# Kernel optimization log

Hardware: AMD Instinct MI355X
Metric: run time of the kernel (lower is better)

## Reference

```python
import jax, jax.numpy as jnp
import numpy as np

BETA = 0.5
TAU_L = 0.1
TAU_H = 0.1
TOP_K = 2


def setup_inputs() -> dict:
    key = jax.random.key(0)
    ks = jax.random.split(key, 6)
    B, S, H, F, E, NH = 1, 2048, 1024, 3584, 8, 16
    hidden_states = jax.random.normal(ks[0], (B, S, H), dtype=jnp.float32)
    self_attn_weights = jax.random.uniform(ks[1], (B, NH, S, S), dtype=jnp.float32)
    gate_w = jax.random.normal(ks[2], (E, H), dtype=jnp.float32) * 0.02
    w1 = jax.random.normal(ks[3], (E, F, H), dtype=jnp.float32) * 0.02
    w2 = jax.random.normal(ks[4], (E, H, F), dtype=jnp.float32) * 0.02
    w3 = jax.random.normal(ks[5], (E, F, H), dtype=jnp.float32) * 0.02
    return {"hidden_states": hidden_states, "self_attn_weights": self_attn_weights,
            "gate_w": gate_w, "w1": w1, "w2": w2, "w3": w3}


def reference(hidden_states, self_attn_weights, gate_w, w1, w2, w3):
    B, S, H = hidden_states.shape
    E = gate_w.shape[0]
    x = hidden_states.reshape(-1, H)          # [T, H], T = B*S
    T = x.shape[0]

    router_logits = x @ gate_w.T              # [T, E]
    rw_full = jax.nn.softmax(router_logits.astype(jnp.float32), axis=-1)
    rw, sel = jax.lax.top_k(rw_full, TOP_K)   # [T, 2]

    # --- dynamic pruning branch (loss_index < block_range) ---
    mask_top1 = rw[:, 1] < BETA * rw[:, 0]
    new_routing = jnp.ones_like(rw)
    new_routing = new_routing.at[:, 1].set(jnp.where(mask_top1, 0.0, 1.0))

    # sequence_length > 1: attention-based token pruning (assumes B == 1)
    mean_tensor = jnp.mean(jnp.squeeze(self_attn_weights), axis=0)  # [S, S]
    column = mean_tensor.shape[1]
    real_number = jnp.arange(column, 0, -1, dtype=jnp.float32)
    attention_scores = jnp.sum(mean_tensor, axis=1) / real_number   # [S]
    l1_norm = jnp.sum(jnp.abs(x), axis=1)                           # [T]
    attention_scores = attention_scores * l1_norm

    n_low = int(TAU_L * T)
    n_high = int(TAU_H * T)
    _, low_idx = jax.lax.top_k(-attention_scores, n_low)   # smallest
    _, high_idx = jax.lax.top_k(attention_scores, n_high)  # largest
    mask_all = jnp.zeros((T,), dtype=bool).at[low_idx].set(True)
    keep_all = jnp.zeros((T,), dtype=bool).at[high_idx].set(True)
    new_routing = jnp.where(mask_all[:, None], 0.0, new_routing)
    new_routing = jnp.where(keep_all[:, None], 1.0, new_routing)

    rw = rw * new_routing
    denom = jnp.sum(rw, axis=-1, keepdims=True)
    rw = rw / jnp.where(denom > 0, denom, 1.0)  # fully-masked tokens -> 0 output
    rw = rw.astype(x.dtype)

    # combine weights per (token, expert); dispatch mask == new_routing
    cw = jnp.sum(rw[:, :, None] * jax.nn.one_hot(sel, E, dtype=rw.dtype), axis=1)  # [T, E]

    # dense reference for the gather-expert-scatter loop (SwiGLU experts)
    h = jnp.einsum('th,efh->tef', x, w1)      # [T, E, F]
    g = jnp.einsum('th,efh->tef', x, w3)
    a = jax.nn.silu(h) * g
    y = jnp.einsum('tef,ehf->teh', a, w2)     # [T, E, H]
    out = jnp.einsum('te,teh->th', cw, y)     # [T, H]

    return out.reshape(B, S, H), router_logits
```

## Files before the change

kernel.cpp:

```cpp
#include <hip/hip_runtime.h>
#include <hip/hip_bf16.h>
#include <math.h>

#define NTOK 2048
#define HDIM 1024
#define NEXP 8
#define FDIM 3584
#define NHEADS 16
#define NLOW 204
#define NHIGH 204
#define BK 32
#define LDST 40
#define KSPLIT 4
#define KCH (FDIM / KSPLIT)

typedef __bf16 bf16x8 __attribute__((ext_vector_type(8)));
typedef float f32x4 __attribute__((ext_vector_type(4)));

__global__ __launch_bounds__(256) void k_xbf16(
    const float* __restrict__ x, __hip_bfloat16* __restrict__ xb)
{
    int i = (blockIdx.x * 256 + threadIdx.x) * 8;
    float4 a = *(const float4*)(x + i);
    float4 b = *(const float4*)(x + i + 4);
    bf16x8 v;
    v[0] = (__bf16)a.x; v[1] = (__bf16)a.y; v[2] = (__bf16)a.z; v[3] = (__bf16)a.w;
    v[4] = (__bf16)b.x; v[5] = (__bf16)b.y; v[6] = (__bf16)b.z; v[7] = (__bf16)b.w;
    *(bf16x8*)(xb + i) = v;
}

__global__ __launch_bounds__(256) void k_router(
    const float* __restrict__ x, const float* __restrict__ gw,
    float* __restrict__ logits, float* __restrict__ l1,
    int* __restrict__ sel0, int* __restrict__ sel1,
    float* __restrict__ rw0, float* __restrict__ rw1)
{
    __shared__ float sgw[NEXP * HDIM];
    int tid = threadIdx.x;
    for (int i = tid; i < NEXP * HDIM; i += 256) sgw[i] = gw[i];
    __syncthreads();
    int wv = tid >> 6, lane = tid & 63;
    int t = blockIdx.x * 4 + wv;
    const float* xr = x + (size_t)t * HDIM;
    float acc[NEXP];
#pragma unroll
    for (int e = 0; e < NEXP; ++e) acc[e] = 0.f;
    float al1 = 0.f;
    for (int h = lane; h < HDIM; h += 64) {
        float xv = xr[h];
        al1 += fabsf(xv);
#pragma unroll
        for (int e = 0; e < NEXP; ++e) acc[e] += xv * sgw[e * HDIM + h];
    }
#pragma unroll
    for (int off = 32; off > 0; off >>= 1) {
#pragma unroll
        for (int e = 0; e < NEXP; ++e) acc[e] += __shfl_xor(acc[e], off);
        al1 += __shfl_xor(al1, off);
    }
    if (lane < NEXP) logits[t * NEXP + lane] = acc[lane];
    if (lane == 0) {
        l1[t] = al1;
        float m = acc[0];
#pragma unroll
        for (int e = 1; e < NEXP; ++e) m = fmaxf(m, acc[e]);
        float p[NEXP], s = 0.f;
#pragma unroll
        for (int e = 0; e < NEXP; ++e) { p[e] = expf(acc[e] - m); s += p[e]; }
        float inv = 1.f / s;
        float b0 = -1.f, b1 = -1.f; int i0 = 0, i1 = 0;
#pragma unroll
        for (int e = 0; e < NEXP; ++e) {
            float r = p[e] * inv;
            if (r > b0) { b1 = b0; i1 = i0; b0 = r; i0 = e; }
            else if (r > b1) { b1 = r; i1 = e; }
        }
        sel0[t] = i0; sel1[t] = i1; rw0[t] = b0; rw1[t] = b1;
    }
}

__global__ __launch_bounds__(256) void k_attn(
    const float* __restrict__ attn, const float* __restrict__ l1,
    float* __restrict__ scores)
{
    int i = blockIdx.x, tid = threadIdx.x;
    float acc = 0.f;
    for (int h = 0; h < NHEADS; ++h) {
        const float4* p = (const float4*)(attn + ((size_t)h * NTOK + i) * NTOK);
        for (int j = tid; j < NTOK / 4; j += 256) {
            float4 v = p[j];
            acc += v.x + v.y + v.z + v.w;
        }
    }
    __shared__ float red[256];
    red[tid] = acc; __syncthreads();
    for (int s = 128; s > 0; s >>= 1) {
        if (tid < s) red[tid] += red[tid + s];
        __syncthreads();
    }
    if (tid == 0) scores[i] = red[0] / (16.f * (float)(NTOK - i)) * l1[i];
}

__global__ __launch_bounds__(256) void k_rank(
    const float* __restrict__ scores, const float* __restrict__ rw0,
    const float* __restrict__ rw1, float* __restrict__ w0f, float* __restrict__ w1f)
{
    __shared__ float s[NTOK];
    int tid = threadIdx.x;
    for (int i = tid; i < NTOK; i += 256) s[i] = scores[i];
    __syncthreads();
    int t = blockIdx.x * 256 + tid;
    float st = s[t];
    int cl = 0, ch = 0;
    for (int j = 0; j < NTOK; ++j) {
        float sj = s[j];
        int tie = (sj == st) && (j < t);
        cl += (sj < st) || tie;
        ch += (sj > st) || tie;
    }
    bool in_low = cl < NLOW, keep = ch < NHIGH;
    float a = rw0[t], b = rw1[t];
    float n0 = 1.f, n1 = (b < 0.5f * a) ? 0.f : 1.f;
    if (in_low) { n0 = 0.f; n1 = 0.f; }
    if (keep)   { n0 = 1.f; n1 = 1.f; }
    a *= n0; b *= n1;
    float d = a + b;
    if (d > 0.f) { a /= d; b /= d; }
    w0f[t] = a; w1f[t] = b;
}

__global__ __launch_bounds__(512) void k_build(
    const int* __restrict__ sel0, const int* __restrict__ sel1,
    const float* __restrict__ w0f, const float* __restrict__ w1f,
    int* __restrict__ tok, float* __restrict__ wgt,
    int* __restrict__ counts, int* __restrict__ offs)
{
    int tid = threadIdx.x;
    int e = tid >> 6, lane = tid & 63;
    unsigned long long below = (1ull << lane) - 1ull;
    int base = 0;
    for (int r = 0; r < NTOK / 64; ++r) {
        int t = r * 64 + lane;
        bool f0 = (sel0[t] == e) && (w0f[t] > 0.f);
        unsigned long long m0 = __ballot(f0);
        if (f0) {
            int pos = base + __popcll(m0 & below);
            tok[e * NTOK + pos] = t; wgt[e * NTOK + pos] = w0f[t];
        }
        base += __popcll(m0);
        bool f1 = (sel1[t] == e) && (w1f[t] > 0.f);
        unsigned long long m1 = __ballot(f1);
        if (f1) {
            int pos = base + __popcll(m1 & below);
            tok[e * NTOK + pos] = t; wgt[e * NTOK + pos] = w1f[t];
        }
        base += __popcll(m1);
    }
    if (lane == 0) counts[e] = base;
    __syncthreads();
    if (tid == 0) {
        int o = 0;
        for (int i = 0; i < NEXP; ++i) { offs[i] = o; o += counts[i]; }
    }
}

__global__ __launch_bounds__(256) void k_zero(float4* __restrict__ out)
{
    out[blockIdx.x * 256 + threadIdx.x] = make_float4(0.f, 0.f, 0.f, 0.f);
}

struct F16v { float4 a, b, c, d; };
__device__ inline F16v ld16(const float* __restrict__ p)
{
    F16v v;
    v.a = *(const float4*)p;
    v.b = *(const float4*)(p + 4);
    v.c = *(const float4*)(p + 8);
    v.d = *(const float4*)(p + 12);
    return v;
}
__device__ inline void st16(__hip_bfloat16* dst, const F16v& v)
{
    bf16x8 lo, hi;
    lo[0] = (__bf16)v.a.x; lo[1] = (__bf16)v.a.y; lo[2] = (__bf16)v.a.z; lo[3] = (__bf16)v.a.w;
    lo[4] = (__bf16)v.b.x; lo[5] = (__bf16)v.b.y; lo[6] = (__bf16)v.b.z; lo[7] = (__bf16)v.b.w;
    hi[0] = (__bf16)v.c.x; hi[1] = (__bf16)v.c.y; hi[2] = (__bf16)v.c.z; hi[3] = (__bf16)v.c.w;
    hi[4] = (__bf16)v.d.x; hi[5] = (__bf16)v.d.y; hi[6] = (__bf16)v.d.z; hi[7] = (__bf16)v.d.w;
    *(bf16x8*)dst = lo;
    *(bf16x8*)(dst + 8) = hi;
}

__global__ __launch_bounds__(256, 2) void k_ffn1(
    const __hip_bfloat16* __restrict__ xb, const float* __restrict__ w1,
    const float* __restrict__ w3,
    const int* __restrict__ tok, const float* __restrict__ wgt,
    const int* __restrict__ counts, const int* __restrict__ offs,
    __hip_bfloat16* __restrict__ act)
{
    int e = blockIdx.z;
    int cnt = counts[e];
    int m0 = blockIdx.y * 128;
    if (m0 >= cnt) return;
    int f0 = blockIdx.x * 128;
    int tid = threadIdx.x;
    __shared__ __align__(16) __hip_bfloat16 sX[2][128 * LDST];
    __shared__ __align__(16) __hip_bfloat16 sW1[2][128 * LDST];
    __shared__ __align__(16) __hip_bfloat16 sW3[2][128 * LDST];
    __shared__ int sTok[128];
    __shared__ float sWgt[128];
    if (tid < 128) {
        int row = m0 + tid;
        int rr = (row < cnt) ? row : (cnt - 1);
        sTok[tid] = tok[e * NTOK + rr];
        sWgt[tid] = (row < cnt) ? wgt[e * NTOK + row] : 0.f;
    }
    __syncthreads();

    int r = tid >> 1, c16 = (tid & 1) * 16;
    const __hip_bfloat16* xp = xb + (size_t)sTok[r] * HDIM + c16;
    const float* w1p = w1 + ((size_t)e * FDIM + f0 + r) * HDIM + c16;
    const float* w3p = w3 + ((size_t)e * FDIM + f0 + r) * HDIM + c16;
    int sidx = r * LDST + c16;

    {
        bf16x8 x0 = *(const bf16x8*)xp, x1 = *(const bf16x8*)(xp + 8);
        F16v w0 = ld16(w1p), g0 = ld16(w3p);
        *(bf16x8*)&sX[0][sidx] = x0;
        *(bf16x8*)&sX[0][sidx + 8] = x1;
        st16(&sW1[0][sidx], w0);
        st16(&sW3[0][sidx], g0);
    }
    __syncthreads();

    int wv = tid >> 6, lane = tid & 63;
    int wm = (wv >> 1) * 64, wf = (wv & 1) * 64;
    int col = lane & 15, kfrag = (lane >> 4) * 8;
    f32x4 acc1[4][4] = {}, acc3[4][4] = {};
    int cur = 0;
    for (int k0 = 0; k0 < HDIM; k0 += BK) {
        bool more = (k0 + BK) < HDIM;
        bf16x8 xn0, xn1; F16v wn, gn;
        if (more) {
            xn0 = *(const bf16x8*)(xp + k0 + BK);
            xn1 = *(const bf16x8*)(xp + k0 + BK + 8);
            wn = ld16(w1p + k0 + BK);
            gn = ld16(w3p + k0 + BK);
        }
        bf16x8 af[4], b1f[4], b3f[4];
#pragma unroll
        for (int m = 0; m < 4; ++m)
            af[m] = *(const bf16x8*)&sX[cur][(wm + m * 16 + col) * LDST + kfrag];
#pragma unroll
        for (int f = 0; f < 4; ++f) {
            b1f[f] = *(const bf16x8*)&sW1[cur][(wf + f * 16 + col) * LDST + kfrag];
            b3f[f] = *(const bf16x8*)&sW3[cur][(wf + f * 16 + col) * LDST + kfrag];
        }
#pragma unroll
        for (int m = 0; m < 4; ++m)
#pragma unroll
            for (int f = 0; f < 4; ++f) {
                acc1[m][f] = __builtin_amdgcn_mfma_f32_16x16x32_bf16(af[m], b1f[f], acc1[m][f], 0, 0, 0);
                acc3[m][f] = __builtin_amdgcn_mfma_f32_16x16x32_bf16(af[m], b3f[f], acc3[m][f], 0, 0, 0);
            }
        if (more) {
            *(bf16x8*)&sX[cur ^ 1][sidx] = xn0;
            *(bf16x8*)&sX[cur ^ 1][sidx + 8] = xn1;
            st16(&sW1[cur ^ 1][sidx], wn);
            st16(&sW3[cur ^ 1][sidx], gn);
        }
        __syncthreads();
        cur ^= 1;
    }
    int soff = offs[e];
#pragma unroll
    for (int m = 0; m < 4; ++m) {
        int mb = wm + m * 16 + (lane >> 4) * 4;
#pragma unroll
        for (int q = 0; q < 4; ++q) {
            int rloc = mb + q;
            if (m0 + rloc < cnt) {
                float wgtv = sWgt[rloc];
#pragma unroll
                for (int f = 0; f < 4; ++f) {
                    float hv = acc1[m][f][q], gv = acc3[m][f][q];
                    float av = hv / (1.f + expf(-hv)) * gv * wgtv;
                    act[(size_t)(soff + m0 + rloc) * FDIM + f0 + wf + f * 16 + col] =
                        (__hip_bfloat16)av;
                }
            }
        }
    }
}

__global__ __launch_bounds__(256, 3) void k_ffn2(
    const __hip_bfloat16* __restrict__ act, const float* __restrict__ w2,
    const int* __restrict__ tok, const int* __restrict__ counts,
    const int* __restrict__ offs, float* __restrict__ out)
{
    int z = blockIdx.z;
    int e = z >> 2;
    int kbase = (z & 3) * KCH;
    int cnt = counts[e];
    int m0 = blockIdx.y * 128;
    if (m0 >= cnt) return;
    int h0 = blockIdx.x * 128;
    int tid = threadIdx.x;
    __shared__ __align__(16) __hip_bfloat16 sA[2][128 * LDST];
    __shared__ __align__(16) __hip_bfloat16 sB[2][128 * LDST];
    __shared__ int sTok[128];
    if (tid < 128) {
        int row = m0 + tid;
        sTok[tid] = (row < cnt) ? tok[e * NTOK + row] : 0;
    }
    __syncthreads();
    int soff = offs[e];
    int r = tid >> 1, c16 = (tid & 1) * 16;
    int arow = (m0 + r < cnt) ? (m0 + r) : (cnt - 1);
    const __hip_bfloat16* ap = act + (size_t)(soff + arow) * FDIM + kbase + c16;
    const float* bp = w2 + ((size_t)e * HDIM + h0 + r) * FDIM + kbase + c16;
    int sidx = r * LDST + c16;

    {
        bf16x8 a0 = *(const bf16x8*)ap, a1 = *(const bf16x8*)(ap + 8);
        F16v b0 = ld16(bp);
        *(bf16x8*)&sA[0][sidx] = a0;
        *(bf16x8*)&sA[0][sidx + 8] = a1;
        st16(&sB[0][sidx], b0);
    }
    __syncthreads();

    int wv = tid >> 6, lane = tid & 63;
    int wm = (wv >> 1) * 64, wh = (wv & 1) * 64;
    int col = lane & 15, kfrag = (lane >> 4) * 8;
    f32x4 acc[4][4] = {};
    int cur = 0;
    for (int k0 = 0; k0 < KCH; k0 += BK) {
        bool more = (k0 + BK) < KCH;
        bf16x8 an0, an1; F16v wn;
        if (more) {
            an0 = *(const bf16x8*)(ap + k0 + BK);
            an1 = *(const bf16x8*)(ap + k0 + BK + 8);
            wn = ld16(bp + k0 + BK);
        }
        bf16x8 aa[4], bb[4];
#pragma unroll
        for (int m = 0; m < 4; ++m)
            aa[m] = *(const bf16x8*)&sA[cur][(wm + m * 16 + col) * LDST + kfrag];
#pragma unroll
        for (int f = 0; f < 4; ++f)
            bb[f] = *(const bf16x8*)&sB[cur][(wh + f * 16 + col) * LDST + kfrag];
#pragma unroll
        for (int m = 0; m < 4; ++m)
#pragma unroll
            for (int f = 0; f < 4; ++f)
                acc[m][f] = __builtin_amdgcn_mfma_f32_16x16x32_bf16(aa[m], bb[f], acc[m][f], 0, 0, 0);
        if (more) {
            *(bf16x8*)&sA[cur ^ 1][sidx] = an0;
            *(bf16x8*)&sA[cur ^ 1][sidx + 8] = an1;
            st16(&sB[cur ^ 1][sidx], wn);
        }
        __syncthreads();
        cur ^= 1;
    }
#pragma unroll
    for (int m = 0; m < 4; ++m) {
        int mb = wm + m * 16 + (lane >> 4) * 4;
#pragma unroll
        for (int q = 0; q < 4; ++q) {
            int rloc = mb + q;
            if (m0 + rloc < cnt) {
                int t = sTok[rloc];
#pragma unroll
                for (int f = 0; f < 4; ++f)
                    atomicAdd(&out[(size_t)t * HDIM + h0 + wh + f * 16 + col], acc[m][f][q]);
            }
        }
    }
}

extern "C" void kernel_launch(void* const* d_in, const int* in_sizes, int n_in,
                              void* d_out, int out_size, void* d_ws, size_t ws_size,
                              hipStream_t stream)
{
    const float* x    = (const float*)d_in[0];
    const float* attn = (const float*)d_in[1];
    const float* gw   = (const float*)d_in[2];
    const float* w1   = (const float*)d_in[3];
    const float* w2   = (const float*)d_in[4];
    const float* w3   = (const float*)d_in[5];
    float* out = (float*)d_out;
    float* logits = out + (size_t)NTOK * HDIM;

    char* ws = (char*)d_ws;
    float* l1     = (float*)(ws + 0);
    float* scores = (float*)(ws + 8192);
    int*   sel0   = (int*)(ws + 16384);
    int*   sel1   = (int*)(ws + 24576);
    float* rw0    = (float*)(ws + 32768);
    float* rw1    = (float*)(ws + 40960);
    float* w0f    = (float*)(ws + 49152);
    float* w1f    = (float*)(ws + 57344);
    int*   counts = (int*)(ws + 65536);
    int*   offs   = (int*)(ws + 65600);
    int*   tok    = (int*)(ws + 73728);
    float* wgt    = (float*)(ws + 143360);
    __hip_bfloat16* act = (__hip_bfloat16*)(ws + 1048576);
    __hip_bfloat16* xb  = (__hip_bfloat16*)(ws + 33554432);

    k_xbf16<<<NTOK * HDIM / (256 * 8), 256, 0, stream>>>(x, xb);
    k_router<<<NTOK / 4, 256, 0, stream>>>(x, gw, logits, l1, sel0, sel1, rw0, rw1);
    k_attn<<<NTOK, 256, 0, stream>>>(attn, l1, scores);
    k_rank<<<NTOK / 256, 256, 0, stream>>>(scores, rw0, rw1, w0f, w1f);
    k_build<<<1, 512, 0, stream>>>(sel0, sel1, w0f, w1f, tok, wgt, counts, offs);
    k_zero<<<NTOK, 256, 0, stream>>>((float4*)out);
    k_ffn1<<<dim3(FDIM / 128, NTOK / 128, NEXP), 256, 0, stream>>>(
        xb, w1, w3, tok, wgt, counts, offs, act);
    k_ffn2<<<dim3(HDIM / 128, NTOK / 128, NEXP * KSPLIT), 256, 0, stream>>>(
        act, w2, tok, counts, offs, out);
}
```

Before: 405.1 us.

## Pre-convert expert weights to bf16 and stage tiles via direct global-to-LDS loads

Adds a per-call pre-pass that converts w1, w3 and w2 from fp32 to bf16 in workspace. The two FFN GEMM kernels now load tiles straight into LDS with global_load_lds using an XOR-swizzled layout, replacing register-staged loads that converted in flight. Tiles become 128x64 with BK=64 and a single LDS buffer, with occupancy hints raised. The conversion passes re-read all expert weights every call (~3x fp32 read plus bf16 write), and the loop no longer double-buffers, so load/compute overlap depends on occupancy.

```diff
diff --git a/kernel.cpp b/kernel.cpp
--- a/kernel.cpp
+++ b/kernel.cpp
@@ -9,13 +9,19 @@
 #define NHEADS 16
 #define NLOW 204
 #define NHIGH 204
-#define BK 32
-#define LDST 40
+#define BK 64
 #define KSPLIT 4
 #define KCH (FDIM / KSPLIT)
 
 typedef __bf16 bf16x8 __attribute__((ext_vector_type(8)));
 typedef float f32x4 __attribute__((ext_vector_type(4)));
+
+__device__ __forceinline__ void gload16(__hip_bfloat16* lds, const __hip_bfloat16* g)
+{
+    __builtin_amdgcn_global_load_lds(
+        (const __attribute__((address_space(1))) unsigned int*)g,
+        (__attribute__((address_space(3))) unsigned int*)lds, 16, 0, 0);
+}
 
 __global__ __launch_bounds__(256) void k_xbf16(
     const float* __restrict__ x, __hip_bfloat16* __restrict__ xb)
@@ -27,6 +33,18 @@
     v[0] = (__bf16)a.x; v[1] = (__bf16)a.y; v[2] = (__bf16)a.z; v[3] = (__bf16)a.w;
     v[4] = (__bf16)b.x; v[5] = (__bf16)b.y; v[6] = (__bf16)b.z; v[7] = (__bf16)b.w;
     *(bf16x8*)(xb + i) = v;
+}
+
+__global__ __launch_bounds__(256) void k_w16(
+    const float* __restrict__ src, __hip_bfloat16* __restrict__ dst)
+{
+    size_t i = ((size_t)blockIdx.x * 256 + threadIdx.x) * 8;
+    float4 a = *(const float4*)(src + i);
+    float4 b = *(const float4*)(src + i + 4);
+    bf16x8 v;
+    v[0] = (__bf16)a.x; v[1] = (__bf16)a.y; v[2] = (__bf16)a.z; v[3] = (__bf16)a.w;
+    v[4] = (__bf16)b.x; v[5] = (__bf16)b.y; v[6] = (__bf16)b.z; v[7] = (__bf16)b.w;
+    *(bf16x8*)(dst + i) = v;
 }
 
 __global__ __launch_bounds__(256) void k_router(
@@ -169,30 +187,9 @@
     out[blockIdx.x * 256 + threadIdx.x] = make_float4(0.f, 0.f, 0.f, 0.f);
 }
 
-struct F16v { float4 a, b, c, d; };
-__device__ inline F16v ld16(const float* __restrict__ p)
-{
-    F16v v;
-    v.a = *(const float4*)p;
-    v.b = *(const float4*)(p + 4);
-    v.c = *(const float4*)(p + 8);
-    v.d = *(const float4*)(p + 12);
-    return v;
-}
-__device__ inline void st16(__hip_bfloat16* dst, const F16v& v)
-{
-    bf16x8 lo, hi;
-    lo[0] = (__bf16)v.a.x; lo[1] = (__bf16)v.a.y; lo[2] = (__bf16)v.a.z; lo[3] = (__bf16)v.a.w;
-    lo[4] = (__bf16)v.b.x; lo[5] = (__bf16)v.b.y; lo[6] = (__bf16)v.b.z; lo[7] = (__bf16)v.b.w;
-    hi[0] = (__bf16)v.c.x; hi[1] = (__bf16)v.c.y; hi[2] = (__bf16)v.c.z; hi[3] = (__bf16)v.c.w;
-    hi[4] = (__bf16)v.d.x; hi[5] = (__bf16)v.d.y; hi[6] = (__bf16)v.d.z; hi[7] = (__bf16)v.d.w;
-    *(bf16x8*)dst = lo;
-    *(bf16x8*)(dst + 8) = hi;
-}
-
-__global__ __launch_bounds__(256, 2) void k_ffn1(
-    const __hip_bfloat16* __restrict__ xb, const float* __restrict__ w1,
-    const float* __restrict__ w3,
+__global__ __launch_bounds__(256, 3) void k_ffn1(
+    const __hip_bfloat16* __restrict__ xb, const __hip_bfloat16* __restrict__ wb1,
+    const __hip_bfloat16* __restrict__ wb3,
     const int* __restrict__ tok, const float* __restrict__ wgt,
     const int* __restrict__ counts, const int* __restrict__ offs,
     __hip_bfloat16* __restrict__ act)
@@ -201,11 +198,11 @@
     int cnt = counts[e];
     int m0 = blockIdx.y * 128;
     if (m0 >= cnt) return;
-    int f0 = blockIdx.x * 128;
+    int f0 = blockIdx.x * 64;
     int tid = threadIdx.x;
-    __shared__ __align__(16) __hip_bfloat16 sX[2][128 * LDST];
-    __shared__ __align__(16) __hip_bfloat16 sW1[2][128 * LDST];
-    __shared__ __align__(16) __hip_bfloat16 sW3[2][128 * LDST];
+    __shared__ __align__(16) __hip_bfloat16 sX[128 * BK];
+    __shared__ __align__(16) __hip_bfloat16 sW1[64 * BK];
+    __shared__ __align__(16) __hip_bfloat16 sW3[64 * BK];
     __shared__ int sTok[128];
     __shared__ float sWgt[128];
     if (tid < 128) {
@@ -216,75 +213,81 @@
     }
     __syncthreads();
 
-    int r = tid >> 1, c16 = (tid & 1) * 16;
-    const __hip_bfloat16* xp = xb + (size_t)sTok[r] * HDIM + c16;
-    const float* w1p = w1 + ((size_t)e * FDIM + f0 + r) * HDIM + c16;
-    const float* w3p = w3 + ((size_t)e * FDIM + f0 + r) * HDIM + c16;
-    int sidx = r * LDST + c16;
-
-    {
-        bf16x8 x0 = *(const bf16x8*)xp, x1 = *(const bf16x8*)(xp + 8);
-        F16v w0 = ld16(w1p), g0 = ld16(w3p);
-        *(bf16x8*)&sX[0][sidx] = x0;
-        *(bf16x8*)&sX[0][sidx + 8] = x1;
-        st16(&sW1[0][sidx], w0);
-        st16(&sW3[0][sidx], g0);
-    }
-    __syncthreads();
-
     int wv = tid >> 6, lane = tid & 63;
-    int wm = (wv >> 1) * 64, wf = (wv & 1) * 64;
-    int col = lane & 15, kfrag = (lane >> 4) * 8;
-    f32x4 acc1[4][4] = {}, acc3[4][4] = {};
-    int cur = 0;
+    int lr = lane >> 3;
+    int sw8 = (((lane & 7) ^ lr) << 3);
+
+    const __hip_bfloat16* gx[4];
+    __hip_bfloat16* lx[4];
+#pragma unroll
+    for (int j = 0; j < 4; ++j) {
+        int c = 4 * wv + j;
+        gx[j] = xb + (size_t)sTok[8 * c + lr] * HDIM + sw8;
+        lx[j] = sX + c * 512;
+    }
+    const __hip_bfloat16* gw1[2]; const __hip_bfloat16* gw3[2];
+    __hip_bfloat16* lw1[2]; __hip_bfloat16* lw3[2];
+#pragma unroll
+    for (int j = 0; j < 2; ++j) {
+        int c = 2 * wv + j;
+        gw1[j] = wb1 + ((size_t)e * FDIM + f0 + 8 * c + lr) * HDIM + sw8;
+        gw3[j] = wb3 + ((size_t)e * FDIM + f0 + 8 * c + lr) * HDIM + sw8;
+        lw1[j] = sW1 + c * 512;
+        lw3[j] = sW3 + c * 512;
+    }
+
+    int colx = lane & 15;
+    int swz = (colx & 7) << 4;
+    int kb0 = (lane >> 4) * 16;
+    f32x4 acc1[2][4] = {}, acc3[2][4] = {};
+
     for (int k0 = 0; k0 < HDIM; k0 += BK) {
-        bool more = (k0 + BK) < HDIM;
-        bf16x8 xn0, xn1; F16v wn, gn;
-        if (more) {
-            xn0 = *(const bf16x8*)(xp + k0 + BK);
-            xn1 = *(const bf16x8*)(xp + k0 + BK + 8);
-            wn = ld16(w1p + k0 + BK);
-            gn = ld16(w3p + k0 + BK);
-        }
-        bf16x8 af[4], b1f[4], b3f[4];
-#pragma unroll
-        for (int m = 0; m < 4; ++m)
-            af[m] = *(const bf16x8*)&sX[cur][(wm + m * 16 + col) * LDST + kfrag];
-#pragma unroll
-        for (int f = 0; f < 4; ++f) {
-            b1f[f] = *(const bf16x8*)&sW1[cur][(wf + f * 16 + col) * LDST + kfrag];
-            b3f[f] = *(const bf16x8*)&sW3[cur][(wf + f * 16 + col) * LDST + kfrag];
-        }
-#pragma unroll
-        for (int m = 0; m < 4; ++m)
+#pragma unroll
+        for (int j = 0; j < 4; ++j) gload16(lx[j], gx[j] + k0);
+#pragma unroll
+        for (int j = 0; j < 2; ++j) {
+            gload16(lw1[j], gw1[j] + k0);
+            gload16(lw3[j], gw3[j] + k0);
+        }
+        __syncthreads();
+#pragma unroll
+        for (int ks = 0; ks < 2; ++ks) {
+            int off = ((kb0 + ks * 64) ^ swz) >> 1;
+            bf16x8 a_[2];
+#pragma unroll
+            for (int m = 0; m < 2; ++m) {
+                int row = 32 * wv + m * 16 + colx;
+                a_[m] = *(const bf16x8*)&sX[(row << 6) + off];
+            }
 #pragma unroll
             for (int f = 0; f < 4; ++f) {
-                acc1[m][f] = __builtin_amdgcn_mfma_f32_16x16x32_bf16(af[m], b1f[f], acc1[m][f], 0, 0, 0);
-                acc3[m][f] = __builtin_amdgcn_mfma_f32_16x16x32_bf16(af[m], b3f[f], acc3[m][f], 0, 0, 0);
-            }
-        if (more) {
-            *(bf16x8*)&sX[cur ^ 1][sidx] = xn0;
-            *(bf16x8*)&sX[cur ^ 1][sidx + 8] = xn1;
-            st16(&sW1[cur ^ 1][sidx], wn);
-            st16(&sW3[cur ^ 1][sidx], gn);
+                int row = f * 16 + colx;
+                bf16x8 b1 = *(const bf16x8*)&sW1[(row << 6) + off];
+                bf16x8 b3 = *(const bf16x8*)&sW3[(row << 6) + off];
+#pragma unroll
+                for (int m = 0; m < 2; ++m) {
+                    acc1[m][f] = __builtin_amdgcn_mfma_f32_16x16x32_bf16(a_[m], b1, acc1[m][f], 0, 0, 0);
+                    acc3[m][f] = __builtin_amdgcn_mfma_f32_16x16x32_bf16(a_[m], b3, acc3[m][f], 0, 0, 0);
+                }
+            }
         }
         __syncthreads();
-        cur ^= 1;
     }
     int soff = offs[e];
-#pragma unroll
-    for (int m = 0; m < 4; ++m) {
-        int mb = wm + m * 16 + (lane >> 4) * 4;
+    int lane4 = (lane >> 4) * 4;
+#pragma unroll
+    for (int m = 0; m < 2; ++m) {
+        int rbase = 32 * wv + m * 16 + lane4;
 #pragma unroll
         for (int q = 0; q < 4; ++q) {
-            int rloc = mb + q;
+            int rloc = rbase + q;
             if (m0 + rloc < cnt) {
                 float wgtv = sWgt[rloc];
 #pragma unroll
                 for (int f = 0; f < 4; ++f) {
                     float hv = acc1[m][f][q], gv = acc3[m][f][q];
                     float av = hv / (1.f + expf(-hv)) * gv * wgtv;
-                    act[(size_t)(soff + m0 + rloc) * FDIM + f0 + wf + f * 16 + col] =
+                    act[(size_t)(soff + m0 + rloc) * FDIM + f0 + f * 16 + colx] =
                         (__hip_bfloat16)av;
                 }
             }
@@ -292,8 +295,8 @@
     }
 }
 
-__global__ __launch_bounds__(256, 3) void k_ffn2(
-    const __hip_bfloat16* __restrict__ act, const float* __restrict__ w2,
+__global__ __launch_bounds__(256, 4) void k_ffn2(
+    const __hip_bfloat16* __restrict__ act, const __hip_bfloat16* __restrict__ wb2,
     const int* __restrict__ tok, const int* __restrict__ counts,
     const int* __restrict__ offs, float* __restrict__ out)
 {
@@ -303,10 +306,10 @@
     int cnt = counts[e];
     int m0 = blockIdx.y * 128;
     if (m0 >= cnt) return;
-    int h0 = blockIdx.x * 128;
+    int h0 = blockIdx.x * 64;
     int tid = threadIdx.x;
-    __shared__ __align__(16) __hip_bfloat16 sA[2][128 * LDST];
-    __shared__ __align__(16) __hip_bfloat16 sB[2][128 * LDST];
+    __shared__ __align__(16) __hip_bfloat16 sA[128 * BK];
+    __shared__ __align__(16) __hip_bfloat16 sB[64 * BK];
     __shared__ int sTok[128];
     if (tid < 128) {
         int row = m0 + tid;
@@ -314,65 +317,72 @@
     }
     __syncthreads();
     int soff = offs[e];
-    int r = tid >> 1, c16 = (tid & 1) * 16;
-    int arow = (m0 + r < cnt) ? (m0 + r) : (cnt - 1);
-    const __hip_bfloat16* ap = act + (size_t)(soff + arow) * FDIM + kbase + c16;
-    const float* bp = w2 + ((size_t)e * HDIM + h0 + r) * FDIM + kbase + c16;
-    int sidx = r * LDST + c16;
-
-    {
-        bf16x8 a0 = *(const bf16x8*)ap, a1 = *(const bf16x8*)(ap + 8);
-        F16v b0 = ld16(bp);
-        *(bf16x8*)&sA[0][sidx] = a0;
-        *(bf16x8*)&sA[0][sidx + 8] = a1;
-        st16(&sB[0][sidx], b0);
-    }
-    __syncthreads();
-
     int wv = tid >> 6, lane = tid & 63;
-    int wm = (wv >> 1) * 64, wh = (wv & 1) * 64;
-    int col = lane & 15, kfrag = (lane >> 4) * 8;
-    f32x4 acc[4][4] = {};
-    int cur = 0;
+    int lr = lane >> 3;
+    int sw8 = (((lane & 7) ^ lr) << 3);
+
+    const __hip_bfloat16* ga[4];
+    __hip_bfloat16* la[4];
+#pragma unroll
+    for (int j = 0; j < 4; ++j) {
+        int c = 4 * wv + j;
+        int trow = 8 * c + lr;
+        int arow = (m0 + trow < cnt) ? (m0 + trow) : (cnt - 1);
+        ga[j] = act + (size_t)(soff + arow) * FDIM + kbase + sw8;
+        la[j] = sA + c * 512;
+    }
+    const __hip_bfloat16* gb[2];
+    __hip_bfloat16* lb[2];
+#pragma unroll
+    for (int j = 0; j < 2; ++j) {
+        int c = 2 * wv + j;
+        gb[j] = wb2 + ((size_t)e * HDIM + h0 + 8 * c + lr) * FDIM + kbase + sw8;
+        lb[j] = sB + c * 512;
+    }
+
+    int colx = lane & 15;
+    int swz = (colx & 7) << 4;
+    int kb0 = (lane >> 4) * 16;
+    f32x4 acc[2][4] = {};
+
     for (int k0 = 0; k0 < KCH; k0 += BK) {
-        bool more = (k0 + BK) < KCH;
-        bf16x8 an0, an1; F16v wn;
-        if (more) {
-            an0 = *(const bf16x8*)(ap + k0 + BK);
-            an1 = *(const bf16x8*)(ap + k0 + BK + 8);
-            wn = ld16(bp + k0 + BK);
-        }
-        bf16x8 aa[4], bb[4];
-#pragma unroll
-        for (int m = 0; m < 4; ++m)
-            aa[m] = *(const bf16x8*)&sA[cur][(wm + m * 16 + col) * LDST + kfrag];
-#pragma unroll
-        for (int f = 0; f < 4; ++f)
-            bb[f] = *(const bf16x8*)&sB[cur][(wh + f * 16 + col) * LDST + kfrag];
-#pragma unroll
-        for (int m = 0; m < 4; ++m)
-#pragma unroll
-            for (int f = 0; f < 4; ++f)
-                acc[m][f] = __builtin_amdgcn_mfma_f32_16x16x32_bf16(aa[m], bb[f], acc[m][f], 0, 0, 0);
-        if (more) {
-            *(bf16x8*)&sA[cur ^ 1][sidx] = an0;
-            *(bf16x8*)&sA[cur ^ 1][sidx + 8] = an1;
-            st16(&sB[cur ^ 1][sidx], wn);
-        }
+#pragma unroll
+        for (int j = 0; j < 4; ++j) gload16(la[j], ga[j] + k0);
+#pragma unroll
+        for (int j = 0; j < 2; ++j) gload16(lb[j], gb[j] + k0);
         __syncthreads();
-        cur ^= 1;
-    }
-#pragma unroll
-    for (int m = 0; m < 4; ++m) {
-        int mb = wm + m * 16 + (lane >> 4) * 4;
+#pragma unroll
+        for (int ks = 0; ks < 2; ++ks) {
+            int off = ((kb0 + ks * 64) ^ swz) >> 1;
+            bf16x8 a_[2];
+#pragma unroll
+            for (int m = 0; m < 2; ++m) {
+                int row = 32 * wv + m * 16 + colx;
+                a_[m] = *(const bf16x8*)&sA[(row << 6) + off];
+            }
+#pragma unroll
+            for (int f = 0; f < 4; ++f) {
+                int row = f * 16 + colx;
+                bf16x8 b = *(const bf16x8*)&sB[(row << 6) + off];
+#pragma unroll
+                for (int m = 0; m < 2; ++m)
+                    acc[m][f] = __builtin_amdgcn_mfma_f32_16x16x32_bf16(a_[m], b, acc[m][f], 0, 0, 0);
+            }
+        }
+        __syncthreads();
+    }
+    int lane4 = (lane >> 4) * 4;
+#pragma unroll
+    for (int m = 0; m < 2; ++m) {
+        int rbase = 32 * wv + m * 16 + lane4;
 #pragma unroll
         for (int q = 0; q < 4; ++q) {
-            int rloc = mb + q;
+            int rloc = rbase + q;
             if (m0 + rloc < cnt) {
                 int t = sTok[rloc];
 #pragma unroll
                 for (int f = 0; f < 4; ++f)
-                    atomicAdd(&out[(size_t)t * HDIM + h0 + wh + f * 16 + col], acc[m][f][q]);
+                    atomicAdd(&out[(size_t)t * HDIM + h0 + f * 16 + colx], acc[m][f][q]);
             }
         }
     }
@@ -406,15 +416,23 @@
     float* wgt    = (float*)(ws + 143360);
     __hip_bfloat16* act = (__hip_bfloat16*)(ws + 1048576);
     __hip_bfloat16* xb  = (__hip_bfloat16*)(ws + 33554432);
+    __hip_bfloat16* wb1 = (__hip_bfloat16*)(ws + 67108864);
+    __hip_bfloat16* wb3 = (__hip_bfloat16*)(ws + 134217728);
+    __hip_bfloat16* wb2 = (__hip_bfloat16*)(ws + 201326592);
+
+    const int NW = NEXP * FDIM * HDIM;
 
     k_xbf16<<<NTOK * HDIM / (256 * 8), 256, 0, stream>>>(x, xb);
+    k_w16<<<NW / (256 * 8), 256, 0, stream>>>(w1, wb1);
+    k_w16<<<NW / (256 * 8), 256, 0, stream>>>(w3, wb3);
+    k_w16<<<NW / (256 * 8), 256, 0, stream>>>(w2, wb2);
     k_router<<<NTOK / 4, 256, 0, stream>>>(x, gw, logits, l1, sel0, sel1, rw0, rw1);
     k_attn<<<NTOK, 256, 0, stream>>>(attn, l1, scores);
     k_rank<<<NTOK / 256, 256, 0, stream>>>(scores, rw0, rw1, w0f, w1f);
     k_build<<<1, 512, 0, stream>>>(sel0, sel1, w0f, w1f, tok, wgt, counts, offs);
     k_zero<<<NTOK, 256, 0, stream>>>((float4*)out);
-    k_ffn1<<<dim3(FDIM / 128, NTOK / 128, NEXP), 256, 0, stream>>>(
-        xb, w1, w3, tok, wgt, counts, offs, act);
-    k_ffn2<<<dim3(HDIM / 128, NTOK / 128, NEXP * KSPLIT), 256, 0, stream>>>(
-        act, w2, tok, counts, offs, out);
-}
+    k_ffn1<<<dim3(FDIM / 64, NTOK / 128, NEXP), 256, 0, stream>>>(
+        xb, wb1, wb3, tok, wgt, counts, offs, act);
+    k_ffn2<<<dim3(HDIM / 64, NTOK / 128, NEXP * KSPLIT), 256, 0, stream>>>(
+        act, wb2, tok, counts, offs, out);
+}
```

Measured after the change: 413.5 us. 2.1% more time.
